# Optimization experiments

Measured on AMD Instinct MI355X. Metric: run time of the kernel, lower is better.

The kernel has to match this reference:

```python
import jax, jax.numpy as jnp
import numpy as np

B, S, H = 32, 2048, 1024

def setup_inputs() -> dict:
    key = jax.random.key(0)
    k0, k1, k2, k3 = jax.random.split(key, 4)
    return {
        "encoder_output": jax.random.normal(k0, (B, S, H), dtype=jnp.float32),
        "target_state": jax.random.normal(k1, (1, B, H), dtype=jnp.float32),
        "Wa_w": jax.random.normal(k2, (H, H), dtype=jnp.float32) / np.float32(np.sqrt(H)),
        "Wc_w": jax.random.normal(k3, (H, 2 * H), dtype=jnp.float32) / np.float32(np.sqrt(2 * H)),
        "Wc_b": jnp.zeros((H,), dtype=jnp.float32),
    }

def reference(encoder_output, target_state, Wa_w, Wc_w, Wc_b):
    # Luong 'general' attention, single decode step.
    state = target_state[0]                                        # [B, H]
    # Wa(encoder_output): Linear without bias -> enc @ Wa_w^T
    proj = jnp.einsum('bsh,gh->bsg', encoder_output, Wa_w)         # [B, S, H]
    attn_score = jnp.einsum('bsh,bh->bs', proj, state)             # [B, S]
    softmax_attn = jax.nn.softmax(attn_score, axis=1)              # [B, S]
    context = jnp.einsum('bs,bsh->bh', softmax_attn, encoder_output)  # [B, H]
    concat = jnp.concatenate([context, state], axis=1)             # [B, 2H]
    # Wc(tanh(concat)) then relu, shape [1, B, H]
    output = jax.nn.relu(jnp.tanh(concat) @ Wc_w.T + Wc_b)[None]
    return output, softmax_attn
```

## Files before the change

### kernel.cpp

```cpp
#include <hip/hip_runtime.h>
#include <math.h>

#define Bdim 32
#define Sdim 2048
#define Hdim 1024

typedef float f4 __attribute__((ext_vector_type(4)));

#define OFF_SCORES 0
#define OFF_U      65536
#define OFF_PM     98304
#define OFF_PL     99328
#define OFF_TC     100352
#define OFF_PACC   165888

__device__ __forceinline__ float dot4(float4 a, float4 b) {
    return a.x*b.x + a.y*b.y + a.z*b.z + a.w*b.w;
}

__global__ void __launch_bounds__(512) k01_u(
        const float* __restrict__ state, const float* __restrict__ Wa,
        float* __restrict__ u) {
    const int hc = blockIdx.x;
    const int b  = blockIdx.y;
    const int t  = threadIdx.x;
    __shared__ float st[1024];
    __shared__ float red[512];
    if (t < 256)
        reinterpret_cast<float4*>(st)[t] =
            reinterpret_cast<const float4*>(state + (size_t)b * Hdim)[t];
    __syncthreads();

    const int h  = hc * 128 + (t & 127);
    const int g0 = (t >> 7) * 256;
    const float* wp = Wa + (size_t)g0 * Hdim + h;
    float acc = 0.f;
#pragma unroll 32
    for (int g = 0; g < 256; ++g)
        acc += st[g0 + g] * wp[(size_t)g * Hdim];
    red[t] = acc;
    __syncthreads();
    if (t < 128)
        u[(size_t)b * Hdim + h] = red[t] + red[t + 128] + red[t + 256] + red[t + 384];
}

__global__ void __launch_bounds__(256) k2_main(
        const float* __restrict__ enc, const float* __restrict__ u,
        float* __restrict__ scores, float* __restrict__ pm,
        float* __restrict__ pl, float* __restrict__ pacc) {
    const int sc   = blockIdx.x;
    const int b    = blockIdx.y;
    const int t    = threadIdx.x;
    const int wv   = t >> 6;
    const int lane = t & 63;

    __shared__ float wm[4], wl[4];
    __shared__ float wacc[4][1024];

    float uf[16];
    const float4* u4 = reinterpret_cast<const float4*>(u + (size_t)b * Hdim);
#pragma unroll
    for (int i = 0; i < 4; ++i) {
        float4 v = u4[i * 64 + lane];
        uf[4*i] = v.x; uf[4*i+1] = v.y; uf[4*i+2] = v.z; uf[4*i+3] = v.w;
    }

    float acc[16];
#pragma unroll
    for (int j = 0; j < 16; ++j) acc[j] = 0.f;
    float m = -INFINITY, l = 0.f;

    const int s0 = sc * 64 + wv * 16;
    const f4* base4 =
        reinterpret_cast<const f4*>(enc + ((size_t)b * Sdim + s0) * Hdim);

    for (int g = 0; g < 8; ++g) {
        float x[2][16];
#pragma unroll
        for (int k = 0; k < 2; ++k) {
            const f4* row4 = base4 + (size_t)(g * 2 + k) * 256;
#pragma unroll
            for (int i = 0; i < 4; ++i) {
                f4 v = row4[i * 64 + lane];
                x[k][4*i] = v.x; x[k][4*i+1] = v.y; x[k][4*i+2] = v.z; x[k][4*i+3] = v.w;
            }
        }
        float d[2];
#pragma unroll
        for (int k = 0; k < 2; ++k) {
            float dd = 0.f;
#pragma unroll
            for (int j = 0; j < 16; ++j) dd += x[k][j] * uf[j];
            d[k] = dd;
        }
#pragma unroll
        for (int off = 32; off >= 1; off >>= 1) {
            d[0] += __shfl_xor(d[0], off, 64);
            d[1] += __shfl_xor(d[1], off, 64);
        }
        if (lane == 0) {
            scores[(size_t)b * Sdim + s0 + g*2 + 0] = d[0];
            scores[(size_t)b * Sdim + s0 + g*2 + 1] = d[1];
        }
        float gm = fmaxf(d[0], d[1]);
        if (gm > m) {
            float al = __expf(m - gm);
#pragma unroll
            for (int j = 0; j < 16; ++j) acc[j] *= al;
            l *= al;
            m = gm;
        }
#pragma unroll
        for (int k = 0; k < 2; ++k) {
            float p = __expf(d[k] - m);
            l += p;
#pragma unroll
            for (int j = 0; j < 16; ++j) acc[j] += p * x[k][j];
        }
    }

    if (lane == 0) { wm[wv] = m; wl[wv] = l; }
    float4* wa = reinterpret_cast<float4*>(&wacc[wv][0]);
#pragma unroll
    for (int i = 0; i < 4; ++i)
        wa[i * 64 + lane] = make_float4(acc[4*i], acc[4*i+1], acc[4*i+2], acc[4*i+3]);
    __syncthreads();

    const float M  = fmaxf(fmaxf(wm[0], wm[1]), fmaxf(wm[2], wm[3]));
    const float e0 = __expf(wm[0] - M), e1 = __expf(wm[1] - M);
    const float e2 = __expf(wm[2] - M), e3 = __expf(wm[3] - M);
    const int pidx = b * 32 + sc;
    if (t == 0) {
        pm[pidx] = M;
        pl[pidx] = e0*wl[0] + e1*wl[1] + e2*wl[2] + e3*wl[3];
    }
    const float4 c0 = *reinterpret_cast<const float4*>(&wacc[0][t * 4]);
    const float4 c1 = *reinterpret_cast<const float4*>(&wacc[1][t * 4]);
    const float4 c2 = *reinterpret_cast<const float4*>(&wacc[2][t * 4]);
    const float4 c3 = *reinterpret_cast<const float4*>(&wacc[3][t * 4]);
    float4 c;
    c.x = e0*c0.x + e1*c1.x + e2*c2.x + e3*c3.x;
    c.y = e0*c0.y + e1*c1.y + e2*c2.y + e3*c3.y;
    c.z = e0*c0.z + e1*c1.z + e2*c2.z + e3*c3.z;
    c.w = e0*c0.w + e1*c1.w + e2*c2.w + e3*c3.w;
    *reinterpret_cast<float4*>(pacc + (size_t)pidx * Hdim + t * 4) = c;
}

__global__ void __launch_bounds__(256) k3_combine(
        const float* __restrict__ pm, const float* __restrict__ pl,
        const float* __restrict__ pacc, const float* __restrict__ scores,
        const float* __restrict__ state,
        float* __restrict__ tc, float* __restrict__ sm_out) {
    const int hq = blockIdx.x;
    const int b  = blockIdx.y;
    const int t  = threadIdx.x;
    __shared__ float e[32];
    __shared__ float MS, LS;
    if (t < 32) {
        float mi = pm[b * 32 + t];
        float M = mi;
#pragma unroll
        for (int off = 16; off >= 1; off >>= 1) M = fmaxf(M, __shfl_xor(M, off, 64));
        float ee = __expf(mi - M);
        float Li = ee * pl[b * 32 + t];
#pragma unroll
        for (int off = 16; off >= 1; off >>= 1) Li += __shfl_xor(Li, off, 64);
        e[t] = ee;
        if (t == 0) { MS = M; LS = Li; }
    }
    __syncthreads();
    const float M = MS, invL = 1.f / LS;

    const int h = hq * 256 + t;
    float c = 0.f;
#pragma unroll 8
    for (int i = 0; i < 32; ++i)
        c += e[i] * pacc[((size_t)(b * 32 + i)) * Hdim + h];
    tc[(size_t)b * 2048 + h] = tanhf(c * invL);
    tc[(size_t)b * 2048 + 1024 + h] = tanhf(state[(size_t)b * Hdim + h]);

#pragma unroll
    for (int i = 0; i < 2; ++i) {
        int s = hq * 512 + i * 256 + t;
        sm_out[(size_t)b * Sdim + s] = __expf(scores[(size_t)b * Sdim + s] - M) * invL;
    }
}

__global__ void __launch_bounds__(256) k4_out(
        const float* __restrict__ tc, const float* __restrict__ Wc,
        const float* __restrict__ Wcb, float* __restrict__ out) {
    const int bx = blockIdx.x;
    const int o0 = (bx >> 1) * 8;
    const int bh = bx & 1;
    const int t  = threadIdx.x;
    const int wv = t >> 6, lane = t & 63;
    const int b0 = bh * 16 + wv * 4;
    const int kb = lane * 4;

    f4 a[4][8];
#pragma unroll
    for (int b = 0; b < 4; ++b)
#pragma unroll
        for (int i = 0; i < 8; ++i)
            a[b][i] = *reinterpret_cast<const f4*>(
                tc + (size_t)(b0 + b) * 2048 + i * 256 + kb);

    float p[8][4];
#pragma unroll
    for (int o = 0; o < 8; ++o) {
        f4 w[8];
#pragma unroll
        for (int i = 0; i < 8; ++i)
            w[i] = *reinterpret_cast<const f4*>(
                Wc + (size_t)(o0 + o) * 2048 + i * 256 + kb);
#pragma unroll
        for (int b = 0; b < 4; ++b) {
            float s = 0.f;
#pragma unroll
            for (int i = 0; i < 8; ++i)
                s += w[i].x*a[b][i].x + w[i].y*a[b][i].y
                   + w[i].z*a[b][i].z + w[i].w*a[b][i].w;
            p[o][b] = s;
        }
    }
#pragma unroll
    for (int off = 32; off >= 1; off >>= 1)
#pragma unroll
        for (int o = 0; o < 8; ++o)
#pragma unroll
            for (int b = 0; b < 4; ++b)
                p[o][b] += __shfl_xor(p[o][b], off, 64);

    if (lane == 0) {
#pragma unroll
        for (int o = 0; o < 8; ++o) {
            float bias = Wcb[o0 + o];
#pragma unroll
            for (int b = 0; b < 4; ++b)
                out[(size_t)(b0 + b) * Hdim + o0 + o] = fmaxf(p[o][b] + bias, 0.f);
        }
    }
}

extern "C" void kernel_launch(void* const* d_in, const int* in_sizes, int n_in,
                              void* d_out, int out_size, void* d_ws, size_t ws_size,
                              hipStream_t stream) {
    const float* enc   = (const float*)d_in[0];
    const float* ts    = (const float*)d_in[1];
    const float* Wa    = (const float*)d_in[2];
    const float* Wc    = (const float*)d_in[3];
    const float* Wcb   = (const float*)d_in[4];
    float* out = (float*)d_out;
    float* ws  = (float*)d_ws;

    float* scores = ws + OFF_SCORES;
    float* u      = ws + OFF_U;
    float* pm     = ws + OFF_PM;
    float* pl     = ws + OFF_PL;
    float* tc     = ws + OFF_TC;
    float* pacc   = ws + OFF_PACC;

    k01_u<<<dim3(8, 32), 512, 0, stream>>>(ts, Wa, u);
    k2_main<<<dim3(32, 32), 256, 0, stream>>>(enc, u, scores, pm, pl, pacc);
    k3_combine<<<dim3(4, 32), 256, 0, stream>>>(pm, pl, pacc, scores, ts,
                                                tc, out + Bdim * Hdim);
    k4_out<<<dim3(256), 256, 0, stream>>>(tc, Wc, Wcb, out);
}
```

Before: 71.75 us.

## Batch state·Wa across all batches with split-K partials and halve main-kernel block size

The u = state·Wa step now computes all 32 batch rows per block over a 32-wide slice of the reduction dimension, so each Wa element is loaded once instead of once per batch. Partial sums go to a workspace buffer and a new combine kernel reduces them. The main attention kernel now uses 128-thread blocks covering 32 sequence rows each, doubling the block count to 2048 and the number of partial softmax states merged in the combine kernel. This removes 32x redundant Wa traffic and adds more parallelism, at the cost of an extra launch and a larger partial-accumulator buffer to read back.

After: 76.73 us. +6.9%, slower.

```diff
diff --git a/kernel.cpp b/kernel.cpp
--- a/kernel.cpp
+++ b/kernel.cpp
@@ -10,41 +10,52 @@
 #define OFF_SCORES 0
 #define OFF_U      65536
 #define OFF_PM     98304
-#define OFF_PL     99328
-#define OFF_TC     100352
-#define OFF_PACC   165888
+#define OFF_PL     100352
+#define OFF_TC     102400
+#define OFF_PACC   167936
+#define OFF_UPART  167936
 
 __device__ __forceinline__ float dot4(float4 a, float4 b) {
     return a.x*b.x + a.y*b.y + a.z*b.z + a.w*b.w;
 }
 
-__global__ void __launch_bounds__(512) k01_u(
+__global__ void __launch_bounds__(128) k0_u_partial(
         const float* __restrict__ state, const float* __restrict__ Wa,
-        float* __restrict__ u) {
+        float* __restrict__ upart) {
+    __shared__ float st[32][32];
     const int hc = blockIdx.x;
-    const int b  = blockIdx.y;
+    const int gc = blockIdx.y;
     const int t  = threadIdx.x;
-    __shared__ float st[1024];
-    __shared__ float red[512];
-    if (t < 256)
-        reinterpret_cast<float4*>(st)[t] =
-            reinterpret_cast<const float4*>(state + (size_t)b * Hdim)[t];
+    for (int i = t; i < 1024; i += 128) {
+        int b = i >> 5, g = i & 31;
+        st[b][g] = state[b * Hdim + gc * 32 + g];
+    }
     __syncthreads();
-
-    const int h  = hc * 128 + (t & 127);
-    const int g0 = (t >> 7) * 256;
-    const float* wp = Wa + (size_t)g0 * Hdim + h;
-    float acc = 0.f;
-#pragma unroll 32
-    for (int g = 0; g < 256; ++g)
-        acc += st[g0 + g] * wp[(size_t)g * Hdim];
-    red[t] = acc;
-    __syncthreads();
-    if (t < 128)
-        u[(size_t)b * Hdim + h] = red[t] + red[t + 128] + red[t + 256] + red[t + 384];
-}
-
-__global__ void __launch_bounds__(256) k2_main(
+    float acc[32];
+#pragma unroll
+    for (int b = 0; b < 32; ++b) acc[b] = 0.f;
+    const int h = hc * 128 + t;
+#pragma unroll
+    for (int g = 0; g < 32; ++g) {
+        float w = Wa[(size_t)(gc * 32 + g) * Hdim + h];
+#pragma unroll
+        for (int b = 0; b < 32; ++b) acc[b] += st[b][g] * w;
+    }
+#pragma unroll
+    for (int b = 0; b < 32; ++b)
+        upart[((size_t)gc * 32 + b) * Hdim + h] = acc[b];
+}
+
+__global__ void __launch_bounds__(256) k1_u_combine(
+        const float* __restrict__ upart, float* __restrict__ u) {
+    const int i = blockIdx.x * 256 + threadIdx.x;
+    float s = 0.f;
+#pragma unroll
+    for (int gc = 0; gc < 32; ++gc) s += upart[(size_t)gc * 32768 + i];
+    u[i] = s;
+}
+
+__global__ void __launch_bounds__(128) k2_main(
         const float* __restrict__ enc, const float* __restrict__ u,
         float* __restrict__ scores, float* __restrict__ pm,
         float* __restrict__ pl, float* __restrict__ pacc) {
@@ -54,8 +65,8 @@
     const int wv   = t >> 6;
     const int lane = t & 63;
 
-    __shared__ float wm[4], wl[4];
-    __shared__ float wacc[4][1024];
+    __shared__ float wm[2], wl[2];
+    __shared__ float wacc[2][1024];
 
     float uf[16];
     const float4* u4 = reinterpret_cast<const float4*>(u + (size_t)b * Hdim);
@@ -70,7 +81,7 @@
     for (int j = 0; j < 16; ++j) acc[j] = 0.f;
     float m = -INFINITY, l = 0.f;
 
-    const int s0 = sc * 64 + wv * 16;
+    const int s0 = sc * 32 + wv * 16;
     const f4* base4 =
         reinterpret_cast<const f4*>(enc + ((size_t)b * Sdim + s0) * Hdim);
 
@@ -126,24 +137,25 @@
         wa[i * 64 + lane] = make_float4(acc[4*i], acc[4*i+1], acc[4*i+2], acc[4*i+3]);
     __syncthreads();
 
-    const float M  = fmaxf(fmaxf(wm[0], wm[1]), fmaxf(wm[2], wm[3]));
+    const float M  = fmaxf(wm[0], wm[1]);
     const float e0 = __expf(wm[0] - M), e1 = __expf(wm[1] - M);
-    const float e2 = __expf(wm[2] - M), e3 = __expf(wm[3] - M);
-    const int pidx = b * 32 + sc;
+    const int pidx = b * 64 + sc;
     if (t == 0) {
         pm[pidx] = M;
-        pl[pidx] = e0*wl[0] + e1*wl[1] + e2*wl[2] + e3*wl[3];
-    }
-    const float4 c0 = *reinterpret_cast<const float4*>(&wacc[0][t * 4]);
-    const float4 c1 = *reinterpret_cast<const float4*>(&wacc[1][t * 4]);
-    const float4 c2 = *reinterpret_cast<const float4*>(&wacc[2][t * 4]);
-    const float4 c3 = *reinterpret_cast<const float4*>(&wacc[3][t * 4]);
-    float4 c;
-    c.x = e0*c0.x + e1*c1.x + e2*c2.x + e3*c3.x;
-    c.y = e0*c0.y + e1*c1.y + e2*c2.y + e3*c3.y;
-    c.z = e0*c0.z + e1*c1.z + e2*c2.z + e3*c3.z;
-    c.w = e0*c0.w + e1*c1.w + e2*c2.w + e3*c3.w;
-    *reinterpret_cast<float4*>(pacc + (size_t)pidx * Hdim + t * 4) = c;
+        pl[pidx] = e0*wl[0] + e1*wl[1];
+    }
+#pragma unroll
+    for (int i = 0; i < 2; ++i) {
+        const int idx = i * 512 + t * 4;
+        const float4 c0 = *reinterpret_cast<const float4*>(&wacc[0][idx]);
+        const float4 c1 = *reinterpret_cast<const float4*>(&wacc[1][idx]);
+        float4 c;
+        c.x = e0*c0.x + e1*c1.x;
+        c.y = e0*c0.y + e1*c1.y;
+        c.z = e0*c0.z + e1*c1.z;
+        c.w = e0*c0.w + e1*c1.w;
+        *reinterpret_cast<float4*>(pacc + (size_t)pidx * Hdim + idx) = c;
+    }
 }
 
 __global__ void __launch_bounds__(256) k3_combine(
@@ -154,17 +166,17 @@
     const int hq = blockIdx.x;
     const int b  = blockIdx.y;
     const int t  = threadIdx.x;
-    __shared__ float e[32];
+    __shared__ float e[64];
     __shared__ float MS, LS;
-    if (t < 32) {
-        float mi = pm[b * 32 + t];
+    if (t < 64) {
+        float mi = pm[b * 64 + t];
         float M = mi;
 #pragma unroll
-        for (int off = 16; off >= 1; off >>= 1) M = fmaxf(M, __shfl_xor(M, off, 64));
+        for (int off = 32; off >= 1; off >>= 1) M = fmaxf(M, __shfl_xor(M, off, 64));
         float ee = __expf(mi - M);
-        float Li = ee * pl[b * 32 + t];
-#pragma unroll
-        for (int off = 16; off >= 1; off >>= 1) Li += __shfl_xor(Li, off, 64);
+        float Li = ee * pl[b * 64 + t];
+#pragma unroll
+        for (int off = 32; off >= 1; off >>= 1) Li += __shfl_xor(Li, off, 64);
         e[t] = ee;
         if (t == 0) { MS = M; LS = Li; }
     }
@@ -174,8 +186,8 @@
     const int h = hq * 256 + t;
     float c = 0.f;
 #pragma unroll 8
-    for (int i = 0; i < 32; ++i)
-        c += e[i] * pacc[((size_t)(b * 32 + i)) * Hdim + h];
+    for (int i = 0; i < 64; ++i)
+        c += e[i] * pacc[((size_t)(b * 64 + i)) * Hdim + h];
     tc[(size_t)b * 2048 + h] = tanhf(c * invL);
     tc[(size_t)b * 2048 + 1024 + h] = tanhf(state[(size_t)b * Hdim + h]);
 
@@ -259,9 +271,11 @@
     float* pl     = ws + OFF_PL;
     float* tc     = ws + OFF_TC;
     float* pacc   = ws + OFF_PACC;
-
-    k01_u<<<dim3(8, 32), 512, 0, stream>>>(ts, Wa, u);
-    k2_main<<<dim3(32, 32), 256, 0, stream>>>(enc, u, scores, pm, pl, pacc);
+    float* upart  = ws + OFF_UPART;
+
+    k0_u_partial<<<dim3(8, 32), 128, 0, stream>>>(ts, Wa, upart);
+    k1_u_combine<<<dim3(128), 256, 0, stream>>>(upart, u);
+    k2_main<<<dim3(64, 32), 128, 0, stream>>>(enc, u, scores, pm, pl, pacc);
     k3_combine<<<dim3(4, 32), 256, 0, stream>>>(pm, pl, pacc, scores, ts,
                                                 tc, out + Bdim * Hdim);
     k4_out<<<dim3(256), 256, 0, stream>>>(tc, Wc, Wcb, out);
```

## Restructure u projection to reuse Wa across batches with split-K partials

Applied to the files above, without the earlier changes.

The state-by-Wa projection is reorganised so each block loads a 32-row slice of Wa once and applies it to all 32 batch rows held in shared memory, writing split-K partial sums. A second small kernel then reduces the 32 partials into u. The old kernel reread the whole Wa matrix once per batch. The new scheme cuts Wa traffic, in exchange for an extra launch and a 4 MB partial buffer that aliases the pacc workspace region.

Measured after the change: 72.78 us. About the same (+1.4%).

```diff
diff --git a/kernel.cpp b/kernel.cpp
--- a/kernel.cpp
+++ b/kernel.cpp
@@ -13,35 +13,46 @@
 #define OFF_PL     99328
 #define OFF_TC     100352
 #define OFF_PACC   165888
+#define OFF_UPART  165888
 
 __device__ __forceinline__ float dot4(float4 a, float4 b) {
     return a.x*b.x + a.y*b.y + a.z*b.z + a.w*b.w;
 }
 
-__global__ void __launch_bounds__(512) k01_u(
+__global__ void __launch_bounds__(128) k0_u_partial(
         const float* __restrict__ state, const float* __restrict__ Wa,
-        float* __restrict__ u) {
+        float* __restrict__ upart) {
+    __shared__ float st[32][32];
     const int hc = blockIdx.x;
-    const int b  = blockIdx.y;
+    const int gc = blockIdx.y;
     const int t  = threadIdx.x;
-    __shared__ float st[1024];
-    __shared__ float red[512];
-    if (t < 256)
-        reinterpret_cast<float4*>(st)[t] =
-            reinterpret_cast<const float4*>(state + (size_t)b * Hdim)[t];
+    for (int i = t; i < 1024; i += 128) {
+        int b = i >> 5, g = i & 31;
+        st[b][g] = state[b * Hdim + gc * 32 + g];
+    }
     __syncthreads();
-
-    const int h  = hc * 128 + (t & 127);
-    const int g0 = (t >> 7) * 256;
-    const float* wp = Wa + (size_t)g0 * Hdim + h;
-    float acc = 0.f;
-#pragma unroll 32
-    for (int g = 0; g < 256; ++g)
-        acc += st[g0 + g] * wp[(size_t)g * Hdim];
-    red[t] = acc;
-    __syncthreads();
-    if (t < 128)
-        u[(size_t)b * Hdim + h] = red[t] + red[t + 128] + red[t + 256] + red[t + 384];
+    float acc[32];
+#pragma unroll
+    for (int b = 0; b < 32; ++b) acc[b] = 0.f;
+    const int h = hc * 128 + t;
+#pragma unroll
+    for (int g = 0; g < 32; ++g) {
+        float w = Wa[(size_t)(gc * 32 + g) * Hdim + h];
+#pragma unroll
+        for (int b = 0; b < 32; ++b) acc[b] += st[b][g] * w;
+    }
+#pragma unroll
+    for (int b = 0; b < 32; ++b)
+        upart[((size_t)gc * 32 + b) * Hdim + h] = acc[b];
+}
+
+__global__ void __launch_bounds__(256) k1_u_combine(
+        const float* __restrict__ upart, float* __restrict__ u) {
+    const int i = blockIdx.x * 256 + threadIdx.x;
+    float s = 0.f;
+#pragma unroll
+    for (int gc = 0; gc < 32; ++gc) s += upart[(size_t)gc * 32768 + i];
+    u[i] = s;
 }
 
 __global__ void __launch_bounds__(256) k2_main(
@@ -259,8 +270,10 @@
     float* pl     = ws + OFF_PL;
     float* tc     = ws + OFF_TC;
     float* pacc   = ws + OFF_PACC;
-
-    k01_u<<<dim3(8, 32), 512, 0, stream>>>(ts, Wa, u);
+    float* upart  = ws + OFF_UPART;
+
+    k0_u_partial<<<dim3(8, 32), 128, 0, stream>>>(ts, Wa, upart);
+    k1_u_combine<<<dim3(128), 256, 0, stream>>>(upart, u);
     k2_main<<<dim3(32, 32), 256, 0, stream>>>(enc, u, scores, pm, pl, pacc);
     k3_combine<<<dim3(4, 32), 256, 0, stream>>>(pm, pl, pacc, scores, ts,
                                                 tc, out + Bdim * Hdim);
```
